# Performance work log

Hardware: AMD Instinct MI355X
Metric: run time of the kernel (lower is better)

## Reference

```python
import jax, jax.numpy as jnp
import numpy as np

N_CLUSTERS = 128
MAX_ITER = 25
MAX_NEIGHBORS = 15
NEG = -1e30  # stand-in for -inf when masking scores


def euc_sim(a, b):
    # 2 a.b - |a|^2 - |b|^2 == -||a-b||^2 ; (n,d),(m,d) -> (n,m)
    return 2.0 * (a @ b.T) - jnp.sum(a * a, axis=1, keepdims=True) - jnp.sum(b * b, axis=1)[None, :]


def fit_predict(pts, ct):
    # sub_sampling=None, lr=1: centroids <- mask@x / (mask.sum+1e-8) each iter.
    # Early tolerance break omitted: with lr=1 the update is a fixed point after
    # convergence, so running the full MAX_ITER iterations yields the same result.
    n = pts.shape[0]
    ones = jnp.ones((n,), pts.dtype)

    def body(i, carry):
        centroids, _ = carry
        sim = euc_sim(pts, centroids)                 # (n, m)
        closest = jnp.argmax(sim, axis=-1)            # (n,)
        sums = jax.ops.segment_sum(pts, closest, num_segments=N_CLUSTERS)   # (m, 3)
        counts = jax.ops.segment_sum(ones, closest, num_segments=N_CLUSTERS)  # (m,)
        new_c = sums / (counts[:, None] + 1e-8)
        return (new_c, closest)

    init = (ct, jnp.zeros((n,), jnp.int32))
    centroids, closest = jax.lax.fori_loop(0, MAX_ITER, body, init)
    # torch returns the assignment computed against the pre-update centroids of
    # the last iteration, exactly what `closest` holds here.
    return closest, centroids


def single_batch(pts, ft, ct):
    closest, centroids = fit_predict(pts, ct)
    sim = euc_sim(pts, centroids)                                  # (n, m)
    in_cluster = closest[:, None] == jnp.arange(N_CLUSTERS)[None, :]
    masked = jnp.where(in_cluster, sim, NEG)                       # (n, m)
    # per-cluster top-k over points; clusters with < K members get NEG slots
    scores, idx = jax.lax.top_k(masked.T, MAX_NEIGHBORS)           # (m, K)
    valid = scores > NEG * 0.5
    smax = jnp.max(jnp.where(valid, scores, NEG), axis=-1, keepdims=True)
    w = jnp.where(valid, jnp.exp(scores - smax), 0.0)
    w = w / jnp.maximum(jnp.sum(w, axis=-1, keepdims=True), 1e-30)  # softmax over valid slots only
    cf = ft[:, idx]                                                # (f, m, K)
    cluster_features = jnp.sum(cf * w[None, :, :], axis=-1)        # (f, m)
    return centroids, cluster_features


def setup_inputs() -> dict:
    key = jax.random.key(0)
    k1, k2, k3 = jax.random.split(key, 3)
    points = jax.random.normal(k1, (4, 100000, 3), jnp.float32)
    features = jax.random.normal(k2, (4, 256, 100000), jnp.float32)
    centroids = jax.random.normal(k3, (4, N_CLUSTERS, 3), jnp.float32)
    return {"points": points, "features": features, "centroids": centroids}


def reference(points, features, centroids):
    # returns (bz x m x 3 cluster centroids, bz x f x m cluster features)
    return jax.vmap(single_batch)(points, features, centroids)
```

## Files before the change

### kernel.cpp

```cpp
#include <hip/hip_runtime.h>
#include <stdint.h>
#include <math.h>

#define B 4
#define N 100000
#define C 128
#define F 256
#define ITERS 25
#define TOPK 15
#define NEGV -1e30f
#define TPB 256
#define NBLK ((N + TPB - 1) / TPB)

__device__ __forceinline__ uint32_t f2u(float f) {
    uint32_t u = __float_as_uint(f);
    return (u & 0x80000000u) ? ~u : (u | 0x80000000u);
}
__device__ __forceinline__ float u2f(uint32_t u) {
    uint32_t bits = (u & 0x80000000u) ? (u & 0x7FFFFFFFu) : ~u;
    return __uint_as_float(bits);
}

__device__ __forceinline__ float sim_np(float x, float y, float z, float an,
                                        float c0, float c1, float c2, float cn) {
    float dot = __fmaf_rn(z, c2, __fmaf_rn(y, c1, __fmul_rn(x, c0)));
    float t = __fmul_rn(2.0f, dot);
    t = __fsub_rn(t, an);
    return __fsub_rn(t, cn);
}
__device__ __forceinline__ float norm3_np(float x, float y, float z) {
    return __fadd_rn(__fadd_rn(__fmul_rn(x, x), __fmul_rn(y, y)), __fmul_rn(z, z));
}

__global__ void k_copyf(const float* __restrict__ src, float* __restrict__ dst, int n) {
    int i = blockIdx.x * blockDim.x + threadIdx.x;
    if (i < n) dst[i] = src[i];
}

__global__ __launch_bounds__(TPB) void k_assign(const float* __restrict__ pts,
        const float* __restrict__ cent, int* __restrict__ closest,
        unsigned char* __restrict__ rank8, unsigned int* __restrict__ blockhist) {
    __shared__ float sc[C * 3];
    __shared__ float cn[C];
    __shared__ unsigned char clid[TPB];
    __shared__ unsigned int hist[C];
    const int b = blockIdx.y;
    const int blk = blockIdx.x;
    const int tid = threadIdx.x;

    for (int i = tid; i < C * 3; i += TPB) sc[i] = cent[b * C * 3 + i];
    if (tid < C) hist[tid] = 0u;
    __syncthreads();
    if (tid < C) cn[tid] = norm3_np(sc[3 * tid], sc[3 * tid + 1], sc[3 * tid + 2]);
    __syncthreads();

    const int p = blk * TPB + tid;
    int bi = 0;
    bool valid = (p < N);
    if (valid) {
        const float* pp = pts + ((size_t)b * N + (size_t)p) * 3;
        float x = pp[0], y = pp[1], z = pp[2];
        float an = norm3_np(x, y, z);
        float best = -INFINITY;
        #pragma unroll 8
        for (int c = 0; c < C; ++c) {
            float s = sim_np(x, y, z, an, sc[3 * c], sc[3 * c + 1], sc[3 * c + 2], cn[c]);
            if (s > best) { best = s; bi = c; }
        }
        closest[b * N + p] = bi;
        clid[tid] = (unsigned char)bi;
        atomicAdd(&hist[bi], 1u);
    } else {
        clid[tid] = 0xFF;
    }
    __syncthreads();
    if (valid) {
        int r = 0;
        #pragma unroll 8
        for (int j = 0; j < tid; ++j) r += (clid[j] == (unsigned char)bi);
        rank8[b * N + p] = (unsigned char)r;
    }
    unsigned int* dst = blockhist + ((size_t)(b * NBLK + blk)) * C;
    for (int i = tid; i < C; i += TPB) dst[i] = hist[i];
}

__global__ __launch_bounds__(128) void k_scan(unsigned int* __restrict__ blockhist,
        unsigned int* __restrict__ cnt, unsigned int* __restrict__ clusterbase) {
    __shared__ unsigned int stot[C];
    __shared__ unsigned int sbase[C];
    const int b = blockIdx.x;
    const int c = threadIdx.x;
    unsigned int run = 0;
    #pragma unroll 4
    for (int i = 0; i < NBLK; ++i) {
        size_t off = ((size_t)(b * NBLK + i)) * C + c;
        unsigned int v = blockhist[off];
        blockhist[off] = run;
        run += v;
    }
    cnt[b * C + c] = run;
    stot[c] = run;
    __syncthreads();
    if (c == 0) {
        unsigned int acc = 0;
        for (int k = 0; k < C; ++k) { sbase[k] = acc; acc += stot[k]; }
    }
    __syncthreads();
    clusterbase[b * C + c] = sbase[c];
}

__global__ __launch_bounds__(TPB) void k_scatter(const int* __restrict__ closest,
        const unsigned char* __restrict__ rank8, const unsigned int* __restrict__ clusterbase,
        const unsigned int* __restrict__ blockbase, unsigned int* __restrict__ ml) {
    const int b = blockIdx.y;
    const int blk = blockIdx.x;
    const int p = blk * TPB + threadIdx.x;
    if (p < N) {
        int c = closest[b * N + p];
        unsigned int pos = clusterbase[b * C + c]
                         + blockbase[((size_t)(b * NBLK + blk)) * C + c]
                         + (unsigned int)rank8[b * N + p];
        ml[(size_t)b * N + pos] = (unsigned int)p;
    }
}

__global__ __launch_bounds__(64) void k_segsum(const float* __restrict__ pts,
        const unsigned int* __restrict__ ml, const unsigned int* __restrict__ clusterbase,
        const unsigned int* __restrict__ cnt, float* __restrict__ cent_next) {
    const int id = blockIdx.x * 64 + threadIdx.x;
    const int b = id / (C * 3);
    const int rem = id % (C * 3);
    const int c = rem / 3;
    const int j = rem % 3;
    const unsigned int base = clusterbase[b * C + c];
    const unsigned int n = cnt[b * C + c];
    const unsigned int* list = ml + (size_t)b * N + base;
    const float* P = pts + (size_t)b * N * 3;
    float s = 0.f;
    unsigned int i = 0;
    for (; i + 32 <= n; i += 32) {
        unsigned int pidx[32];
        #pragma unroll
        for (int u = 0; u < 32; ++u) pidx[u] = list[i + u];
        float t[32];
        #pragma unroll
        for (int u = 0; u < 32; ++u) t[u] = P[pidx[u] * 3 + j];
        #pragma unroll
        for (int u = 0; u < 32; ++u) s = __fadd_rn(s, t[u]);
    }
    for (; i < n; ++i) s = __fadd_rn(s, P[list[i] * 3 + j]);
    float denom = __fadd_rn((float)n, 1e-8f);
    cent_next[(b * C + c) * 3 + j] = __fdiv_rn(s, denom);
}

__global__ __launch_bounds__(TPB) void k_topk(const unsigned int* __restrict__ ml,
        const unsigned int* __restrict__ clusterbase, const unsigned int* __restrict__ cnt,
        const float* __restrict__ pts, const float* __restrict__ cent,
        int* __restrict__ tk_idx, float* __restrict__ tk_w) {
    const int b = blockIdx.y;
    const int c = blockIdx.x;
    const int tid = threadIdx.x;
    const unsigned int base = clusterbase[b * C + c];
    const unsigned int n = cnt[b * C + c];
    const unsigned int* list = ml + (size_t)b * N + base;
    const float* P = pts + (size_t)b * N * 3;

    const float c0 = cent[(b * C + c) * 3 + 0];
    const float c1 = cent[(b * C + c) * 3 + 1];
    const float c2 = cent[(b * C + c) * 3 + 2];
    const float cnorm = norm3_np(c0, c1, c2);

    unsigned long long a[TOPK];
    #pragma unroll
    for (int i = 0; i < TOPK; ++i) a[i] = 0ull;

    for (unsigned int i = tid; i < n; i += TPB) {
        unsigned int p = list[i];
        float x = P[p * 3 + 0], y = P[p * 3 + 1], z = P[p * 3 + 2];
        float an = norm3_np(x, y, z);
        float s = sim_np(x, y, z, an, c0, c1, c2, cnorm);
        unsigned long long key = ((unsigned long long)f2u(s) << 32) | (uint32_t)(~p);
        if (key > a[0]) {
            a[0] = key;
            #pragma unroll
            for (int j = 0; j < TOPK - 1; ++j) {
                if (a[j] > a[j + 1]) {
                    unsigned long long t = a[j]; a[j] = a[j + 1]; a[j + 1] = t;
                }
            }
        }
    }

    __shared__ unsigned long long wred[4];
    __shared__ unsigned long long sel;
    __shared__ unsigned long long res[TOPK];
    const int lane = tid & 63;
    const int wid = tid >> 6;

    for (int r = 0; r < TOPK; ++r) {
        unsigned long long m = a[TOPK - 1];
        #pragma unroll
        for (int off = 32; off >= 1; off >>= 1) {
            unsigned long long o = __shfl_xor(m, off, 64);
            if (o > m) m = o;
        }
        if (lane == 0) wred[wid] = m;
        __syncthreads();
        if (tid == 0) {
            unsigned long long g = wred[0];
            #pragma unroll
            for (int w = 1; w < 4; ++w) if (wred[w] > g) g = wred[w];
            sel = g;
            res[r] = g;
        }
        __syncthreads();
        if (sel != 0ull && a[TOPK - 1] == sel) {
            #pragma unroll
            for (int j = TOPK - 1; j > 0; --j) a[j] = a[j - 1];
            a[0] = 0ull;
        }
    }

    if (tid == 0) {
        float s_[TOPK]; int id_[TOPK];
        for (int i = 0; i < TOPK; ++i) {
            unsigned long long g = res[i];
            if (g == 0ull) { s_[i] = NEGV; id_[i] = 0; }
            else { s_[i] = u2f((uint32_t)(g >> 32)); id_[i] = (int)(~(uint32_t)g); }
        }
        float smax = (s_[0] > 0.5f * NEGV) ? s_[0] : NEGV;
        float w[TOPK]; float sum = 0.f;
        for (int i = 0; i < TOPK; ++i) {
            bool valid = s_[i] > 0.5f * NEGV;
            w[i] = valid ? expf(__fsub_rn(s_[i], smax)) : 0.f;
            sum = __fadd_rn(sum, w[i]);
        }
        float den = fmaxf(sum, 1e-30f);
        for (int i = 0; i < TOPK; ++i) {
            tk_idx[((size_t)b * C + c) * TOPK + i] = id_[i];
            tk_w [((size_t)b * C + c) * TOPK + i] = __fdiv_rn(w[i], den);
        }
    }
}

__global__ __launch_bounds__(128) void k_feat(const float* __restrict__ ft,
        const int* __restrict__ tk_idx, const float* __restrict__ tk_w,
        float* __restrict__ out_cf) {
    const int b = blockIdx.y;
    const int f = blockIdx.x;
    const int c = threadIdx.x;
    __shared__ int sid[C * TOPK];
    __shared__ float sw[C * TOPK];
    for (int i = c; i < C * TOPK; i += 128) {
        sid[i] = tk_idx[(size_t)b * C * TOPK + i];
        sw[i]  = tk_w [(size_t)b * C * TOPK + i];
    }
    __syncthreads();
    const float* row = ft + (size_t)b * F * N + (size_t)f * N;
    float acc = 0.f;
    #pragma unroll
    for (int k = 0; k < TOPK; ++k) {
        acc = __fmaf_rn(sw[c * TOPK + k], row[sid[c * TOPK + k]], acc);
    }
    out_cf[((size_t)b * F + f) * C + c] = acc;
}

extern "C" void kernel_launch(void* const* d_in, const int* in_sizes, int n_in,
                              void* d_out, int out_size, void* d_ws, size_t ws_size,
                              hipStream_t stream) {
    (void)in_sizes; (void)n_in; (void)out_size; (void)ws_size;
    const float* pts = (const float*)d_in[0];
    const float* ft  = (const float*)d_in[1];
    const float* ct0 = (const float*)d_in[2];
    float* out = (float*)d_out;

    float* ws = (float*)d_ws;
    float* centA = ws;
    float* centB = centA + B * C * 3;
    float* tk_w = centB + B * C * 3;
    int* tk_idx = (int*)(tk_w + B * C * TOPK);
    int* closest = tk_idx + B * C * TOPK;
    unsigned int* cnt = (unsigned int*)(closest + (size_t)B * N);
    unsigned int* clusterbase = cnt + B * C;
    unsigned int* ml = clusterbase + B * C;
    unsigned int* blockhist = ml + (size_t)B * N;
    unsigned char* rank8 = (unsigned char*)(blockhist + (size_t)B * NBLK * C);

    const float* cur = ct0;
    float* nxt = centA;
    for (int t = 0; t < ITERS; ++t) {
        k_assign <<<dim3(NBLK, B), dim3(TPB), 0, stream>>>(pts, cur, closest, rank8, blockhist);
        k_scan   <<<dim3(B),       dim3(128), 0, stream>>>(blockhist, cnt, clusterbase);
        k_scatter<<<dim3(NBLK, B), dim3(TPB), 0, stream>>>(closest, rank8, clusterbase, blockhist, ml);
        k_segsum <<<dim3(24),      dim3(64),  0, stream>>>(pts, ml, clusterbase, cnt, nxt);
        cur = nxt;
        nxt = (nxt == centA) ? centB : centA;
    }
    k_topk<<<dim3(C, B), dim3(TPB), 0, stream>>>(ml, clusterbase, cnt, pts, cur, tk_idx, tk_w);
    k_feat<<<dim3(F, B), dim3(128), 0, stream>>>(ft, tk_idx, tk_w, out + B * C * 3);
    k_copyf<<<dim3((B * C * 3 + 255) / 256), dim3(256), 0, stream>>>(cur, out, B * C * 3);
}
```

Before: 4.329 ms.

## Fuse k-means iterations into one cooperative persistent kernel with grid syncs

Replaces the per-iteration launches of assign, scan, scatter and segment-sum with a single cooperative kernel that loops over all iterations, separating phases with grid-wide syncs. Within-block rank is computed with wavefront ballots instead of a quadratic shared-memory loop. The per-cluster block-prefix scan is parallelized across blocks with shared-memory scans rather than a serial walk over 4 blocks. This removes about a hundred kernel launches and the serial scan, at the cost of grid.sync overhead and a fixed 512-block grid.

```diff
diff --git a/kernel.cpp b/kernel.cpp
--- a/kernel.cpp
+++ b/kernel.cpp
@@ -1,6 +1,9 @@
 #include <hip/hip_runtime.h>
+#include <hip/hip_cooperative_groups.h>
 #include <stdint.h>
 #include <math.h>
+
+namespace cg = cooperative_groups;
 
 #define B 4
 #define N 100000
@@ -11,6 +14,7 @@
 #define NEGV -1e30f
 #define TPB 256
 #define NBLK ((N + TPB - 1) / TPB)
+#define GRID 512
 
 __device__ __forceinline__ uint32_t f2u(float f) {
     uint32_t u = __float_as_uint(f);
@@ -37,120 +41,163 @@
     if (i < n) dst[i] = src[i];
 }
 
-__global__ __launch_bounds__(TPB) void k_assign(const float* __restrict__ pts,
-        const float* __restrict__ cent, int* __restrict__ closest,
-        unsigned char* __restrict__ rank8, unsigned int* __restrict__ blockhist) {
-    __shared__ float sc[C * 3];
-    __shared__ float cn[C];
-    __shared__ unsigned char clid[TPB];
-    __shared__ unsigned int hist[C];
-    const int b = blockIdx.y;
-    const int blk = blockIdx.x;
+__global__ __launch_bounds__(TPB, 2) void k_fused(
+        const float* __restrict__ pts, const float* __restrict__ ct0,
+        float* centA, float* centB,
+        unsigned char* __restrict__ cl8, unsigned char* __restrict__ rank8,
+        unsigned int* __restrict__ tilehist, unsigned int* __restrict__ cnt,
+        unsigned int* __restrict__ clusterbase, unsigned int* __restrict__ ml) {
+    cg::grid_group grid = cg::this_grid();
     const int tid = threadIdx.x;
-
-    for (int i = tid; i < C * 3; i += TPB) sc[i] = cent[b * C * 3 + i];
-    if (tid < C) hist[tid] = 0u;
-    __syncthreads();
-    if (tid < C) cn[tid] = norm3_np(sc[3 * tid], sc[3 * tid + 1], sc[3 * tid + 2]);
-    __syncthreads();
-
-    const int p = blk * TPB + tid;
-    int bi = 0;
-    bool valid = (p < N);
-    if (valid) {
-        const float* pp = pts + ((size_t)b * N + (size_t)p) * 3;
-        float x = pp[0], y = pp[1], z = pp[2];
-        float an = norm3_np(x, y, z);
-        float best = -INFINITY;
-        #pragma unroll 8
-        for (int c = 0; c < C; ++c) {
-            float s = sim_np(x, y, z, an, sc[3 * c], sc[3 * c + 1], sc[3 * c + 2], cn[c]);
-            if (s > best) { best = s; bi = c; }
-        }
-        closest[b * N + p] = bi;
-        clid[tid] = (unsigned char)bi;
-        atomicAdd(&hist[bi], 1u);
-    } else {
-        clid[tid] = 0xFF;
-    }
-    __syncthreads();
-    if (valid) {
-        int r = 0;
-        #pragma unroll 8
-        for (int j = 0; j < tid; ++j) r += (clid[j] == (unsigned char)bi);
-        rank8[b * N + p] = (unsigned char)r;
-    }
-    unsigned int* dst = blockhist + ((size_t)(b * NBLK + blk)) * C;
-    for (int i = tid; i < C; i += TPB) dst[i] = hist[i];
-}
-
-__global__ __launch_bounds__(128) void k_scan(unsigned int* __restrict__ blockhist,
-        unsigned int* __restrict__ cnt, unsigned int* __restrict__ clusterbase) {
-    __shared__ unsigned int stot[C];
-    __shared__ unsigned int sbase[C];
-    const int b = blockIdx.x;
-    const int c = threadIdx.x;
-    unsigned int run = 0;
-    #pragma unroll 4
-    for (int i = 0; i < NBLK; ++i) {
-        size_t off = ((size_t)(b * NBLK + i)) * C + c;
-        unsigned int v = blockhist[off];
-        blockhist[off] = run;
-        run += v;
-    }
-    cnt[b * C + c] = run;
-    stot[c] = run;
-    __syncthreads();
-    if (c == 0) {
-        unsigned int acc = 0;
-        for (int k = 0; k < C; ++k) { sbase[k] = acc; acc += stot[k]; }
-    }
-    __syncthreads();
-    clusterbase[b * C + c] = sbase[c];
-}
-
-__global__ __launch_bounds__(TPB) void k_scatter(const int* __restrict__ closest,
-        const unsigned char* __restrict__ rank8, const unsigned int* __restrict__ clusterbase,
-        const unsigned int* __restrict__ blockbase, unsigned int* __restrict__ ml) {
-    const int b = blockIdx.y;
-    const int blk = blockIdx.x;
-    const int p = blk * TPB + threadIdx.x;
-    if (p < N) {
-        int c = closest[b * N + p];
-        unsigned int pos = clusterbase[b * C + c]
-                         + blockbase[((size_t)(b * NBLK + blk)) * C + c]
-                         + (unsigned int)rank8[b * N + p];
-        ml[(size_t)b * N + pos] = (unsigned int)p;
-    }
-}
-
-__global__ __launch_bounds__(64) void k_segsum(const float* __restrict__ pts,
-        const unsigned int* __restrict__ ml, const unsigned int* __restrict__ clusterbase,
-        const unsigned int* __restrict__ cnt, float* __restrict__ cent_next) {
-    const int id = blockIdx.x * 64 + threadIdx.x;
-    const int b = id / (C * 3);
-    const int rem = id % (C * 3);
-    const int c = rem / 3;
-    const int j = rem % 3;
-    const unsigned int base = clusterbase[b * C + c];
-    const unsigned int n = cnt[b * C + c];
-    const unsigned int* list = ml + (size_t)b * N + base;
-    const float* P = pts + (size_t)b * N * 3;
-    float s = 0.f;
-    unsigned int i = 0;
-    for (; i + 32 <= n; i += 32) {
-        unsigned int pidx[32];
-        #pragma unroll
-        for (int u = 0; u < 32; ++u) pidx[u] = list[i + u];
-        float t[32];
-        #pragma unroll
-        for (int u = 0; u < 32; ++u) t[u] = P[pidx[u] * 3 + j];
-        #pragma unroll
-        for (int u = 0; u < 32; ++u) s = __fadd_rn(s, t[u]);
-    }
-    for (; i < n; ++i) s = __fadd_rn(s, P[list[i] * 3 + j]);
-    float denom = __fadd_rn((float)n, 1e-8f);
-    cent_next[(b * C + c) * 3 + j] = __fdiv_rn(s, denom);
+    const int bid = blockIdx.x;
+    const int lane = tid & 63;
+    const int wid = tid >> 6;
+
+    __shared__ float4 scn[C];
+    __shared__ unsigned int wavecnt[4][C];
+    __shared__ unsigned int sscan[2 * TPB];
+
+    for (int t = 0; t < ITERS; ++t) {
+        const float* cur = (t == 0) ? ct0 : ((t & 1) ? centA : centB);
+        float* nxt = (t & 1) ? centB : centA;
+
+        for (int tile = bid; tile < B * NBLK; tile += GRID) {
+            const int b = tile / NBLK;
+            const int blk = tile % NBLK;
+            if (tid < C) {
+                float c0 = cur[(b * C + tid) * 3 + 0];
+                float c1 = cur[(b * C + tid) * 3 + 1];
+                float c2 = cur[(b * C + tid) * 3 + 2];
+                scn[tid] = make_float4(c0, c1, c2, norm3_np(c0, c1, c2));
+            }
+            for (int i = tid; i < 4 * C; i += TPB) ((unsigned int*)wavecnt)[i] = 0u;
+            __syncthreads();
+
+            const int p = blk * TPB + tid;
+            const bool valid = (p < N);
+            int bi = 0;
+            if (valid) {
+                const float* pp = pts + ((size_t)b * N + (size_t)p) * 3;
+                float x = pp[0], y = pp[1], z = pp[2];
+                float an = norm3_np(x, y, z);
+                float best = -INFINITY;
+                #pragma unroll 4
+                for (int c = 0; c < C; ++c) {
+                    float4 cc = scn[c];
+                    float s = sim_np(x, y, z, an, cc.x, cc.y, cc.z, cc.w);
+                    if (s > best) { best = s; bi = c; }
+                }
+            }
+            unsigned long long same = ~0ull;
+            #pragma unroll
+            for (int bit = 0; bit < 7; ++bit) {
+                unsigned long long bb = __ballot((bi >> bit) & 1);
+                same &= ((bi >> bit) & 1) ? bb : ~bb;
+            }
+            unsigned long long vmask = __ballot(valid);
+            same &= vmask;
+            unsigned long long lt = (lane == 0) ? 0ull : (~0ull >> (64 - lane));
+            int rin = (int)__popcll(same & lt);
+            if (valid) {
+                int leader = (int)__builtin_ctzll(same);
+                if (lane == leader) wavecnt[wid][bi] = (unsigned int)__popcll(same);
+            }
+            __syncthreads();
+            if (valid) {
+                int r = rin;
+                #pragma unroll
+                for (int w = 0; w < 4; ++w) if (w < wid) r += wavecnt[w][bi];
+                cl8[(size_t)b * N + p] = (unsigned char)bi;
+                rank8[(size_t)b * N + p] = (unsigned char)r;
+            }
+            if (tid < C) {
+                unsigned int h = wavecnt[0][tid] + wavecnt[1][tid]
+                               + wavecnt[2][tid] + wavecnt[3][tid];
+                tilehist[((size_t)(b * NBLK + blk)) * C + tid] = h;
+            }
+            __syncthreads();
+        }
+        grid.sync();
+
+        for (int chain = bid; chain < B * C; chain += GRID) {
+            const int b = chain / C;
+            const int c = chain % C;
+            unsigned int* th = tilehist + (size_t)b * NBLK * C + c;
+            sscan[tid]       = (tid < NBLK)       ? th[(size_t)tid * C]         : 0u;
+            sscan[tid + TPB] = (tid + TPB < NBLK) ? th[(size_t)(tid + TPB) * C] : 0u;
+            __syncthreads();
+            for (int off = 1; off < 2 * TPB; off <<= 1) {
+                unsigned int a0 = sscan[tid], a1 = sscan[tid + TPB];
+                unsigned int b0 = (tid >= off) ? sscan[tid - off] : 0u;
+                unsigned int b1 = (tid + TPB >= off) ? sscan[tid + TPB - off] : 0u;
+                __syncthreads();
+                sscan[tid] = a0 + b0; sscan[tid + TPB] = a1 + b1;
+                __syncthreads();
+            }
+            if (tid < NBLK)       th[(size_t)tid * C]         = (tid == 0) ? 0u : sscan[tid - 1];
+            if (tid + TPB < NBLK) th[(size_t)(tid + TPB) * C] = sscan[tid + TPB - 1];
+            if (tid == 0) cnt[b * C + c] = sscan[NBLK - 1];
+            __syncthreads();
+        }
+        grid.sync();
+
+        for (int tile = bid; tile < B * NBLK; tile += GRID) {
+            const int b = tile / NBLK;
+            const int blk = tile % NBLK;
+            if (tid < C) sscan[tid] = cnt[b * C + tid];
+            __syncthreads();
+            for (int off = 1; off < C; off <<= 1) {
+                unsigned int a = 0, bb = 0;
+                if (tid < C) { a = sscan[tid]; bb = (tid >= off) ? sscan[tid - off] : 0u; }
+                __syncthreads();
+                if (tid < C) sscan[tid] = a + bb;
+                __syncthreads();
+            }
+            const int p = blk * TPB + tid;
+            if (p < N) {
+                int c = cl8[(size_t)b * N + p];
+                unsigned int cb = (c == 0) ? 0u : sscan[c - 1];
+                unsigned int pos = cb
+                                 + tilehist[((size_t)(b * NBLK + blk)) * C + c]
+                                 + (unsigned int)rank8[(size_t)b * N + p];
+                ml[(size_t)b * N + pos] = (unsigned int)p;
+            }
+            __syncthreads();
+        }
+        grid.sync();
+
+        {
+            const int id = bid * TPB + tid;
+            if (id < B * C * 3) {
+                const int b = id / (C * 3);
+                const int rem = id % (C * 3);
+                const int c = rem / 3;
+                const int j = rem % 3;
+                unsigned int base = 0;
+                for (int k = 0; k < c; ++k) base += cnt[b * C + k];
+                if (j == 0) clusterbase[b * C + c] = base;
+                const unsigned int n = cnt[b * C + c];
+                const unsigned int* list = ml + (size_t)b * N + base;
+                const float* P = pts + (size_t)b * N * 3;
+                float s = 0.f;
+                unsigned int i = 0;
+                for (; i + 32 <= n; i += 32) {
+                    unsigned int pidx[32];
+                    #pragma unroll
+                    for (int u = 0; u < 32; ++u) pidx[u] = list[i + u];
+                    float tv[32];
+                    #pragma unroll
+                    for (int u = 0; u < 32; ++u) tv[u] = P[pidx[u] * 3 + j];
+                    #pragma unroll
+                    for (int u = 0; u < 32; ++u) s = __fadd_rn(s, tv[u]);
+                }
+                for (; i < n; ++i) s = __fadd_rn(s, P[list[i] * 3 + j]);
+                float denom = __fadd_rn((float)n, 1e-8f);
+                nxt[(b * C + c) * 3 + j] = __fdiv_rn(s, denom);
+            }
+        }
+        grid.sync();
+    }
 }
 
 __global__ __launch_bounds__(TPB) void k_topk(const unsigned int* __restrict__ ml,
@@ -279,24 +326,19 @@
     float* centB = centA + B * C * 3;
     float* tk_w = centB + B * C * 3;
     int* tk_idx = (int*)(tk_w + B * C * TOPK);
-    int* closest = tk_idx + B * C * TOPK;
-    unsigned int* cnt = (unsigned int*)(closest + (size_t)B * N);
+    unsigned int* cnt = (unsigned int*)(tk_idx + B * C * TOPK);
     unsigned int* clusterbase = cnt + B * C;
     unsigned int* ml = clusterbase + B * C;
-    unsigned int* blockhist = ml + (size_t)B * N;
-    unsigned char* rank8 = (unsigned char*)(blockhist + (size_t)B * NBLK * C);
-
-    const float* cur = ct0;
-    float* nxt = centA;
-    for (int t = 0; t < ITERS; ++t) {
-        k_assign <<<dim3(NBLK, B), dim3(TPB), 0, stream>>>(pts, cur, closest, rank8, blockhist);
-        k_scan   <<<dim3(B),       dim3(128), 0, stream>>>(blockhist, cnt, clusterbase);
-        k_scatter<<<dim3(NBLK, B), dim3(TPB), 0, stream>>>(closest, rank8, clusterbase, blockhist, ml);
-        k_segsum <<<dim3(24),      dim3(64),  0, stream>>>(pts, ml, clusterbase, cnt, nxt);
-        cur = nxt;
-        nxt = (nxt == centA) ? centB : centA;
-    }
-    k_topk<<<dim3(C, B), dim3(TPB), 0, stream>>>(ml, clusterbase, cnt, pts, cur, tk_idx, tk_w);
+    unsigned int* tilehist = ml + (size_t)B * N;
+    unsigned char* cl8 = (unsigned char*)(tilehist + (size_t)B * NBLK * C);
+    unsigned char* rank8 = cl8 + (size_t)B * N;
+
+    void* args[] = { (void*)&pts, (void*)&ct0, (void*)&centA, (void*)&centB,
+                     (void*)&cl8, (void*)&rank8, (void*)&tilehist, (void*)&cnt,
+                     (void*)&clusterbase, (void*)&ml };
+    hipLaunchCooperativeKernel((void*)k_fused, dim3(GRID), dim3(TPB), args, 0, stream);
+
+    k_topk<<<dim3(C, B), dim3(TPB), 0, stream>>>(ml, clusterbase, cnt, pts, centA, tk_idx, tk_w);
     k_feat<<<dim3(F, B), dim3(128), 0, stream>>>(ft, tk_idx, tk_w, out + B * C * 3);
-    k_copyf<<<dim3((B * C * 3 + 255) / 256), dim3(256), 0, stream>>>(cur, out, B * C * 3);
-}
+    k_copyf<<<dim3((B * C * 3 + 255) / 256), dim3(256), 0, stream>>>(centA, out, B * C * 3);
+}
```

Measured after the change: 9.643 ms. +122.7%, slower.
